# Kernel optimization log

Measured on AMD Instinct MI355X. Metric: run time of the kernel, lower is better.

## Reference

```python
import jax, jax.numpy as jnp
import numpy as np

N_VIEWS = 64
IU0, IU1 = np.triu_indices(N_VIEWS, k=1)  # pair indices (i<j), P = 2016
ALPHA_THRESH = 20.0 / 90.0


def _normal(x, sigma, expo):
    # exp(-x^e / (2*sigma^2))
    return jnp.exp(-jnp.power(x, expo) / (2.0 * sigma * sigma))


def setup_inputs() -> dict:
    key = jax.random.key(0)
    k0, k1, k2 = jax.random.split(key, 3)
    B, P = 4096, N_VIEWS * (N_VIEWS - 1) // 2
    views = jax.random.normal(k0, (B, N_VIEWS, 7), dtype=jnp.float32)
    views = views.at[:, :, 0].set(1.0)  # validity flag compared against ==1
    view_pairs = jax.random.uniform(k1, (B, P, 3), dtype=jnp.float32)
    point_attribute = jax.random.normal(k2, (B, 2), dtype=jnp.float32)
    return {
        "views": views,
        "view_pairs": view_pairs,
        "point_attribute": point_attribute,
        "alpha_sigma1": jnp.float32(5.0 / 90.0),
        "alpha_sigma2": jnp.float32(30.0 / 90.0),
        "gsd_sigma": jnp.float32(1.5),
        "scale_sigma": jnp.float32(0.25),
        "normal_sigma": jnp.float32(30.0 / 90.0),
        "distortion_sigma": jnp.float32(1.0),
    }


def reference(views, view_pairs, point_attribute, alpha_sigma1, alpha_sigma2,
              gsd_sigma, scale_sigma, normal_sigma, distortion_sigma):
    mask = (views[:, :, 0] == 1).astype(views.dtype)            # [B, N]
    pair_mask = (view_pairs[:, :, 0] != 0).astype(views.dtype)  # [B, P]

    a = view_pairs[:, :, 1]
    # step sigma/exponent: zeros_like then fill per threshold (== case stays 0)
    sig = jnp.where(a < ALPHA_THRESH, alpha_sigma1,
                    jnp.where(a > ALPHA_THRESH, alpha_sigma2, 0.0))
    expo = jnp.where(a != ALPHA_THRESH, 2.0, 0.0)
    base_score = _normal(a, sig, expo) * pair_mask               # [B, P]

    gsd = _normal(views[:, :, 4], gsd_sigma, 4.0) * mask         # [B, N]
    scale_score = _normal(view_pairs[:, :, 2], scale_sigma, 2.0) * pair_mask
    nrm = _normal(views[:, :, 5], normal_sigma, 2.0) * mask
    dist = _normal(views[:, :, 6], distortion_sigma, 2.0) * mask

    # Original builds [B,N,N] outer products, triu-masks, gathers upper tri.
    # Equivalent: gather (i,j) pairs directly -> per-pair products, no NxN alloc.
    final = (base_score * scale_score
             * gsd[:, IU0] * gsd[:, IU1]
             * nrm[:, IU0] * nrm[:, IU1]
             * dist[:, IU0] * dist[:, IU1])                      # [B, P]
    return jnp.sum(final, axis=1)                                # [B]
```

## Files before the change

kernel.cpp:

```cpp
#include <hip/hip_runtime.h>

#define NV 64
#define NP 2016
#define NT 504
#define ALPHA_T (20.0f / 90.0f)

__global__ __launch_bounds__(256) void score_kernel(
    const float* __restrict__ views,
    const float* __restrict__ pairs,
    const float* __restrict__ s_a1,
    const float* __restrict__ s_a2,
    const float* __restrict__ s_gsd,
    const float* __restrict__ s_scale,
    const float* __restrict__ s_nrm,
    const float* __restrict__ s_dist,
    float* __restrict__ out)
{
    const int b = blockIdx.x;
    const int t = threadIdx.x;

    __shared__ float gv[NV];
    __shared__ float wsum[4];

    const float a1 = s_a1[0];
    const float a2 = s_a2[0];
    const float gsd_s   = s_gsd[0];
    const float scale_s = s_scale[0];
    const float nrm_s   = s_nrm[0];
    const float dist_s  = s_dist[0];

    const float ia1     = 0.5f / (a1 * a1);
    const float ia2     = 0.5f / (a2 * a2);
    const float c_gsd   = 0.5f / (gsd_s * gsd_s);
    const float c_scale = 0.5f / (scale_s * scale_s);
    const float c_nrm   = 0.5f / (nrm_s * nrm_s);
    const float c_dist  = 0.5f / (dist_s * dist_s);

    if (t < NV) {
        const float* vb = views + ((size_t)b * NV + t) * 7;
        float m  = (vb[0] == 1.0f) ? 1.0f : 0.0f;
        float x4 = vb[4], x5 = vb[5], x6 = vb[6];
        float x4sq = x4 * x4;
        float e = x4sq * x4sq * c_gsd + x5 * x5 * c_nrm + x6 * x6 * c_dist;
        gv[t] = m * __expf(-e);
    }
    __syncthreads();

    const float4* pb4 = (const float4*)(pairs + (size_t)b * NP * 3);
    float acc = 0.0f;

    for (int task = t; task < NT; task += 256) {
        float4 q0 = pb4[3 * task + 0];
        float4 q1 = pb4[3 * task + 1];
        float4 q2 = pb4[3 * task + 2];

        int p = 4 * task;
        int i = (int)((127.0f - sqrtf((float)(16129 - 8 * p))) * 0.5f);
        int Si = (i * (127 - i)) >> 1;
        if (Si > p) { --i; Si = (i * (127 - i)) >> 1; }
        else {
            int Si1 = ((i + 1) * (126 - i)) >> 1;
            if (Si1 <= p) { i = i + 1; Si = Si1; }
        }
        int j = i + 1 + (p - Si);

        const float pm[4] = {q0.x, q0.w, q1.z, q2.y};
        const float av[4] = {q0.y, q1.x, q1.w, q2.z};
        const float sv[4] = {q0.z, q1.y, q2.x, q2.w};

        #pragma unroll
        for (int u = 0; u < 4; ++u) {
            float a = av[u], s = sv[u];
            float coef = (a < ALPHA_T) ? ia1 : ia2;
            float base = __expf(-(a * a * coef + s * s * c_scale));
            if (a == ALPHA_T) base = 0.0f;
            float v = base * gv[i] * gv[j];
            acc += (pm[u] != 0.0f) ? v : 0.0f;
            ++j;
            if (j >= NV) { ++i; j = i + 1; }
        }
    }

    #pragma unroll
    for (int off = 32; off > 0; off >>= 1)
        acc += __shfl_down(acc, off, 64);

    const int wid  = t >> 6;
    const int lane = t & 63;
    if (lane == 0) wsum[wid] = acc;
    __syncthreads();
    if (t == 0) out[b] = wsum[0] + wsum[1] + wsum[2] + wsum[3];
}

extern "C" void kernel_launch(void* const* d_in, const int* in_sizes, int n_in,
                              void* d_out, int out_size, void* d_ws, size_t ws_size,
                              hipStream_t stream) {
    const float* views = (const float*)d_in[0];
    const float* pairs = (const float*)d_in[1];
    const float* a1    = (const float*)d_in[3];
    const float* a2    = (const float*)d_in[4];
    const float* gsd   = (const float*)d_in[5];
    const float* scale = (const float*)d_in[6];
    const float* nrm   = (const float*)d_in[7];
    const float* dist  = (const float*)d_in[8];
    float* out = (float*)d_out;

    const int B = in_sizes[0] / (NV * 7);

    score_kernel<<<B, 256, 0, stream>>>(views, pairs, a1, a2, gsd, scale, nrm, dist, out);
}
```

Baseline: 161.5 us.

## Split into per-view precompute kernel and flat grid-stride pair kernel with atomics

Per-view gaussian factors are now computed by a separate kernel into workspace, which also zeroes the output. A second kernel then processes all pair-tasks over a flat grid-stride index with a fixed grid of 2048 blocks. Each task reads the per-view factors from global memory, and per-batch sums are formed with wave reductions and atomicAdd. This removes the tail imbalance of the old one-block-per-batch layout, where 504 tasks ran on 256 threads, and avoids the per-block shared-memory setup. The cost is a second kernel launch, scattered global loads of the factors, and atomics, which make the float summation order nondeterministic.

```diff
diff --git a/kernel.cpp b/kernel.cpp
--- a/kernel.cpp
+++ b/kernel.cpp
@@ -4,6 +4,106 @@
 #define NP 2016
 #define NT 504
 #define ALPHA_T (20.0f / 90.0f)
+
+__global__ __launch_bounds__(256) void gv_kernel(
+    const float* __restrict__ views,
+    const float* __restrict__ s_gsd,
+    const float* __restrict__ s_nrm,
+    const float* __restrict__ s_dist,
+    float* __restrict__ gvw,
+    float* __restrict__ out,
+    int B)
+{
+    const int tid = blockIdx.x * 256 + threadIdx.x;
+    if (tid < B) out[tid] = 0.0f;
+    const int n = B * NV;
+    if (tid >= n) return;
+
+    const float gsd_s = s_gsd[0], nrm_s = s_nrm[0], dist_s = s_dist[0];
+    const float c_gsd  = 0.5f / (gsd_s * gsd_s);
+    const float c_nrm  = 0.5f / (nrm_s * nrm_s);
+    const float c_dist = 0.5f / (dist_s * dist_s);
+
+    const float* vb = views + (size_t)tid * 7;
+    float m  = (vb[0] == 1.0f) ? 1.0f : 0.0f;
+    float x4 = vb[4], x5 = vb[5], x6 = vb[6];
+    float x4sq = x4 * x4;
+    gvw[tid] = m * __expf(-(x4sq * x4sq * c_gsd + x5 * x5 * c_nrm + x6 * x6 * c_dist));
+}
+
+__global__ __launch_bounds__(256) void pair_kernel(
+    const float* __restrict__ pairs,
+    const float* __restrict__ gvw,
+    const float* __restrict__ s_a1,
+    const float* __restrict__ s_a2,
+    const float* __restrict__ s_scale,
+    float* __restrict__ out,
+    int ntot)
+{
+    const int g    = blockIdx.x * 256 + threadIdx.x;
+    const int S    = gridDim.x * 256;
+    const int lane = threadIdx.x & 63;
+
+    const float a1 = s_a1[0], a2 = s_a2[0], sc = s_scale[0];
+    const float ia1     = 0.5f / (a1 * a1);
+    const float ia2     = 0.5f / (a2 * a2);
+    const float c_scale = 0.5f / (sc * sc);
+
+    const float4* __restrict__ f4 = (const float4*)pairs;
+
+    const int nit = (ntot + S - 1) / S;
+    for (int it = 0; it < nit; ++it) {
+        int task = g + it * S;
+        const bool ok = task < ntot;
+        const int tc = ok ? task : (ntot - 1);
+
+        float4 q0 = f4[3 * tc + 0];
+        float4 q1 = f4[3 * tc + 1];
+        float4 q2 = f4[3 * tc + 2];
+
+        int b = tc / NT;
+        int p = 4 * (tc - b * NT);
+
+        int i = (int)((127.0f - sqrtf((float)(16129 - 8 * p))) * 0.5f);
+        int Si = (i * (127 - i)) >> 1;
+        if (Si > p) { --i; Si = (i * (127 - i)) >> 1; }
+        else {
+            int Si1 = ((i + 1) * (126 - i)) >> 1;
+            if (Si1 <= p) { i = i + 1; Si = Si1; }
+        }
+        int j = i + 1 + (p - Si);
+
+        const float pm[4] = {q0.x, q0.w, q1.z, q2.y};
+        const float av[4] = {q0.y, q1.x, q1.w, q2.z};
+        const float sv[4] = {q0.z, q1.y, q2.x, q2.w};
+
+        const float* gvb = gvw + (b << 6);
+        float acc = 0.0f;
+        #pragma unroll
+        for (int u = 0; u < 4; ++u) {
+            float a = av[u], s = sv[u];
+            float coef = (a < ALPHA_T) ? ia1 : ia2;
+            float base = __expf(-(a * a * coef + s * s * c_scale));
+            if (a == ALPHA_T) base = 0.0f;
+            float v = base * gvb[i] * gvb[j];
+            acc += (pm[u] != 0.0f) ? v : 0.0f;
+            ++j;
+            if (j >= NV) { ++i; j = i + 1; }
+        }
+        if (!ok) acc = 0.0f;
+
+        const int b0 = __shfl(b, 0, 64);
+        float s0 = (b == b0) ? acc : 0.0f;
+        float s1 = (b == b0) ? 0.0f : acc;
+        #pragma unroll
+        for (int off = 32; off > 0; off >>= 1) {
+            s0 += __shfl_xor(s0, off, 64);
+            s1 += __shfl_xor(s1, off, 64);
+        }
+        if (lane == 0 && s0 != 0.0f) atomicAdd(&out[b0], s0);
+        if (lane == 63 && b != b0 && s1 != 0.0f) atomicAdd(&out[b], s1);
+    }
+}
 
 __global__ __launch_bounds__(256) void score_kernel(
     const float* __restrict__ views,
@@ -107,5 +207,13 @@
 
     const int B = in_sizes[0] / (NV * 7);
 
-    score_kernel<<<B, 256, 0, stream>>>(views, pairs, a1, a2, gsd, scale, nrm, dist, out);
-}
+    if (d_ws != nullptr && ws_size >= (size_t)B * NV * sizeof(float)) {
+        float* gvw = (float*)d_ws;
+        const int nviews = B * NV;
+        gv_kernel<<<(nviews + 255) / 256, 256, 0, stream>>>(views, gsd, nrm, dist, gvw, out, B);
+        const int ntot = B * NT;
+        pair_kernel<<<2048, 256, 0, stream>>>(pairs, gvw, a1, a2, scale, out, ntot);
+    } else {
+        score_kernel<<<B, 256, 0, stream>>>(views, pairs, a1, a2, gsd, scale, nrm, dist, out);
+    }
+}
```

Result: no change. 163.6 us (+1.3%).
